# Kernel tuning notes

Hardware: AMD Instinct MI355X
Metric: run time of the kernel (lower is better)

The kernel has to match this reference:

```python
import jax, jax.numpy as jnp
import numpy as np

N_NODES = 50000


def setup_inputs() -> dict:
    key = jax.random.key(0)
    k1, k2, k3, k4, k5 = jax.random.split(key, 5)
    N, E, D_IN, D_OUT = N_NODES, 800000, 128, 128
    features = jax.random.normal(k1, (N, D_IN), dtype=jnp.float32)
    src = jax.random.randint(k2, (E,), 0, N, dtype=jnp.int32)
    dst = jax.random.randint(k3, (E,), 0, N, dtype=jnp.int32)
    # Kaiming-ish init for linear weights
    W_self = jax.random.normal(k4, (D_IN, D_OUT), dtype=jnp.float32) / np.sqrt(D_IN)
    W_neigh = jax.random.normal(k5, (D_IN, D_OUT), dtype=jnp.float32) / np.sqrt(D_IN)
    b = jnp.zeros((D_OUT,), dtype=jnp.float32)
    return {"features": features, "src": src, "dst": dst,
            "W_self": W_self, "W_neigh": W_neigh, "b": b}


def reference(features, src, dst, W_self, W_neigh, b):
    # DGL SAGEConv with 'mean' aggregator:
    #   h_neigh[v] = mean_{(u->v) in E} features[u]   (0 if in-degree 0)
    #   out = features @ W_self + h_neigh @ W_neigh + b
    N = features.shape[0]
    # gather source features along edges, then segment-sum into destinations
    neigh_sum = jax.ops.segment_sum(features[src], dst, num_segments=N)  # [N, D]
    deg = jax.ops.segment_sum(jnp.ones_like(dst, dtype=features.dtype), dst,
                              num_segments=N)  # [N]
    h_neigh = neigh_sum / jnp.maximum(deg, 1.0)[:, None]
    return features @ W_self + h_neigh @ W_neigh + b
```

## Files before the change

kernel.cpp:

```cpp
#include <hip/hip_runtime.h>

#define D 128
#define CAPN 64
#define HPAD 136
#define EC 2048
#define BSH 8
#define CAP 5120
#define CSTR 16

typedef __attribute__((ext_vector_type(8))) short bf16x8;
typedef __attribute__((ext_vector_type(4))) float f32x4;
typedef __attribute__((ext_vector_type(2))) float f32x2;

__device__ __forceinline__ unsigned short f2bf(float f) {
    union { float f; unsigned int u; } c;
    c.f = f;
    unsigned int lsb = (c.u >> 16) & 1u;
    c.u += 0x7fffu + lsb;
    return (unsigned short)(c.u >> 16);
}

__device__ __forceinline__ float bf_lo(unsigned int x) {
    union { unsigned int u; float f; } c;
    c.u = x << 16;
    return c.f;
}
__device__ __forceinline__ float bf_hi(unsigned int x) {
    union { unsigned int u; float f; } c;
    c.u = x & 0xffff0000u;
    return c.f;
}

__global__ __launch_bounds__(256) void prep_kernel(const float* __restrict__ feat,
                                                   unsigned short* __restrict__ fb,
                                                   unsigned char* __restrict__ fq,
                                                   const float* __restrict__ Ws,
                                                   const float* __restrict__ Wn,
                                                   unsigned short* __restrict__ Wfrag,
                                                   int* __restrict__ bin_cursor,
                                                   int castB, int n8, int N) {
    int bid = blockIdx.x;
    int t   = threadIdx.x;
    if (bid < castB) {
        int i = bid * 256 + t;
        if (i >= n8) return;
        const float4* s = (const float4*)(feat + (size_t)i * 8);
        float4 a = s[0];
        float4 b = s[1];
        unsigned short pk[8];
        pk[0] = f2bf(a.x); pk[1] = f2bf(a.y); pk[2] = f2bf(a.z); pk[3] = f2bf(a.w);
        pk[4] = f2bf(b.x); pk[5] = f2bf(b.y); pk[6] = f2bf(b.z); pk[7] = f2bf(b.w);
        *(bf16x8*)(fb + (size_t)i * 8) = *(const bf16x8*)pk;
        unsigned int q0 = __builtin_amdgcn_cvt_pk_fp8_f32(a.x, a.y, 0u, false);
        q0 = __builtin_amdgcn_cvt_pk_fp8_f32(a.z, a.w, q0, true);
        unsigned int q1 = __builtin_amdgcn_cvt_pk_fp8_f32(b.x, b.y, 0u, false);
        q1 = __builtin_amdgcn_cvt_pk_fp8_f32(b.z, b.w, q1, true);
        uint2 qq; qq.x = q0; qq.y = q1;
        *(uint2*)(fq + (size_t)i * 8) = qq;
    } else if (bid < castB + 16) {
        int tid = (bid - castB) * 256 + t;
        int l  = tid & 63;
        int ks = (tid >> 6) & 7;
        int nt = tid >> 9;
        int n  = nt * 16 + (l & 15);
        int kb = ks * 32 + (l >> 4) * 8;
        unsigned short pk[8];
#pragma unroll
        for (int j = 0; j < 8; ++j) {
            int k = kb + j;
            float w = (k < 128) ? Ws[k * D + n] : Wn[(k - 128) * D + n];
            pk[j] = f2bf(w);
        }
        *(bf16x8*)(Wfrag + (size_t)tid * 8) = *(const bf16x8*)pk;
    } else {
#pragma unroll
        for (int j = 0; j < CSTR; ++j)
            bin_cursor[j * 256 + t] = 0;
        if (t < 64)
            ((unsigned int*)(fb + (size_t)N * D))[t] = 0;
        if (t < 32)
            ((unsigned int*)(fq + (size_t)N * D))[t] = 0;
    }
}

__global__ __launch_bounds__(256) void binscatter_kernel(const int* __restrict__ src,
                                                         const int* __restrict__ dst,
                                                         int* __restrict__ bin_cursor,
                                                         unsigned int* __restrict__ ebuf,
                                                         int E, int NB) {
    __shared__ int cnt[256];
    __shared__ int basev[256];
    __shared__ int cur[256];
    int t = threadIdx.x;
    cnt[t] = 0;
    cur[t] = 0;
    __syncthreads();
    int base = blockIdx.x * EC;
    int dr[EC / 256];
#pragma unroll
    for (int i = 0; i < EC / 256; ++i) {
        int e = base + i * 256 + t;
        dr[i] = (e < E) ? dst[e] : -1;
        if (dr[i] >= 0) atomicAdd(&cnt[dr[i] >> BSH], 1);
    }
    __syncthreads();
    if (t < NB && cnt[t]) basev[t] = atomicAdd(&bin_cursor[t * CSTR], cnt[t]);
    __syncthreads();
#pragma unroll
    for (int i = 0; i < EC / 256; ++i) {
        int e = base + i * 256 + t;
        if (dr[i] >= 0) {
            int d = dr[i];
            int b = d >> BSH;
            int loc = basev[b] + atomicAdd(&cur[b], 1);
            if (loc < CAP)
                ebuf[(size_t)b * CAP + loc] =
                    (unsigned int)src[e] | ((unsigned int)(d & ((1 << BSH) - 1)) << 16);
        }
    }
}

__global__ __launch_bounds__(256) void csrbin_kernel(const unsigned int* __restrict__ ebuf,
                                                     const int* __restrict__ bin_cursor,
                                                     int* __restrict__ deg_g,
                                                     unsigned short* __restrict__ bucket,
                                                     int N) {
    __shared__ unsigned short lb[256 * CAPN];
    __shared__ int degL[256];
    int b = blockIdx.x;
    int t = threadIdx.x;
    int cntb = bin_cursor[b * CSTR];
    if (cntb > CAP) cntb = CAP;
    int s  = b * CAP;
    int e2 = s + cntb;

    degL[t] = 0;
    __syncthreads();

    for (int i = s + t; i < e2; i += 256) {
        unsigned int p = ebuf[i];
        int dl = (p >> 16) & 255;
        int slot = atomicAdd(&degL[dl], 1);
        if (slot < CAPN)
            lb[dl * CAPN + slot] = (unsigned short)(p & 0xffffu);
    }
    __syncthreads();

    int node = (b << BSH) + t;
    if (node < N) deg_g[node] = degL[t];

    uint4* dstq = (uint4*)(bucket + (size_t)b * 256 * CAPN);
    const uint4* srcq = (const uint4*)lb;
#pragma unroll
    for (int k = 0; k < (256 * CAPN) / 8 / 256; ++k)
        dstq[k * 256 + t] = srcq[k * 256 + t];
}

__global__ __launch_bounds__(256) void gather_mfma_kernel(
        const unsigned short* __restrict__ fb,
        const unsigned char* __restrict__ fq,
        const unsigned short* __restrict__ bucket,
        const int* __restrict__ deg,
        const unsigned short* __restrict__ Wfrag,
        const float* __restrict__ bias,
        float* __restrict__ out, int N) {
    __shared__ unsigned short hL[16 * HPAD];

    int t    = threadIdx.x;
    int w    = t >> 6;
    int lane = t & 63;
    int half = lane >> 5;
    int c32  = lane & 31;
    int lo16 = lane & 15;
    int quad = lane >> 4;
    int v0   = blockIdx.x * 16;
    int n0   = v0 + w * 4;

    int rowA = v0 + lo16;
    if (rowA > N - 1) rowA = N - 1;
    bf16x8 aself[4];
#pragma unroll
    for (int ks = 0; ks < 4; ++ks)
        aself[ks] = *(const bf16x8*)(fb + (size_t)rowA * D + ks * 32 + quad * 8);

    int nd = n0 + (lane & 3);
    int dn = (nd < N) ? deg[nd] : 0;
    int idx0 = (n0 + 0 < N) ? (int)bucket[(size_t)(n0 + 0) * CAPN + lane] : 0;
    int idx1 = (n0 + 1 < N) ? (int)bucket[(size_t)(n0 + 1) * CAPN + lane] : 0;
    int idx2 = (n0 + 2 < N) ? (int)bucket[(size_t)(n0 + 2) * CAPN + lane] : 0;
    int idx3 = (n0 + 3 < N) ? (int)bucket[(size_t)(n0 + 3) * CAPN + lane] : 0;

    int dt0 = __shfl(dn, 0), dt1 = __shfl(dn, 1);
    int dt2 = __shfl(dn, 2), dt3 = __shfl(dn, 3);
    int d0 = (n0 + 0 < N) ? ((dt0 > CAPN) ? CAPN : dt0) : 0;
    int d1 = (n0 + 1 < N) ? ((dt1 > CAPN) ? CAPN : dt1) : 0;
    int d2 = (n0 + 2 < N) ? ((dt2 > CAPN) ? CAPN : dt2) : 0;
    int d3 = (n0 + 3 < N) ? ((dt3 > CAPN) ? CAPN : dt3) : 0;

    unsigned int xA[16], xB[16];

#define ISSUE(X, idxreg, dd, e0)                                              \
    {                                                                         \
        _Pragma("unroll")                                                     \
        for (int j = 0; j < 16; ++j) {                                        \
            int sl = __builtin_amdgcn_readlane(idxreg, (e0) + 2 * j);         \
            int sh = __builtin_amdgcn_readlane(idxreg, (e0) + 2 * j + 1);     \
            sl = ((e0) + 2 * j     < (dd)) ? sl : N;                          \
            sh = ((e0) + 2 * j + 1 < (dd)) ? sh : N;                          \
            int ue = half ? sh : sl;                                          \
            X[j] = *(const unsigned int*)(fq + (size_t)ue * D + c32 * 4);     \
        }                                                                     \
    }

#define ACCUM(X)                                                              \
    {                                                                         \
        _Pragma("unroll")                                                     \
        for (int j = 0; j < 16; ++j) {                                        \
            f32x2 lo = __builtin_amdgcn_cvt_pk_f32_fp8(X[j], false);          \
            f32x2 hi = __builtin_amdgcn_cvt_pk_f32_fp8(X[j], true);           \
            a0 += lo.x; a1 += lo.y; a2 += hi.x; a3 += hi.y;                   \
        }                                                                     \
    }

#define FINISH(X, idxreg, dd, dtrue, nn)                                      \
    {                                                                         \
        float a0 = 0.f, a1 = 0.f, a2 = 0.f, a3 = 0.f;                         \
        ACCUM(X);                                                             \
        for (int e0 = 32; e0 < (dd); e0 += 32) {                              \
            ISSUE(X, idxreg, dd, e0);                                         \
            ACCUM(X);                                                         \
        }                                                                     \
        a0 += __shfl_xor(a0, 32);                                             \
        a1 += __shfl_xor(a1, 32);                                             \
        a2 += __shfl_xor(a2, 32);                                             \
        a3 += __shfl_xor(a3, 32);                                             \
        if (lane < 32) {                                                      \
            float inv = ((dd) > 0) ? 1.0f / (float)(dtrue) : 0.0f;            \
            uint2 pk;                                                         \
            pk.x = ((unsigned int)f2bf(a1 * inv) << 16) | f2bf(a0 * inv);     \
            pk.y = ((unsigned int)f2bf(a3 * inv) << 16) | f2bf(a2 * inv);     \
            *(uint2*)&hL[(w * 4 + (nn)) * HPAD + c32 * 4] = pk;               \
        }                                                                     \
    }

    ISSUE(xA, idx0, d0, 0);
    ISSUE(xB, idx1, d1, 0);
    FINISH(xA, idx0, d0, dt0, 0);
    ISSUE(xA, idx2, d2, 0);
    FINISH(xB, idx1, d1, dt1, 1);
    ISSUE(xB, idx3, d3, 0);
    FINISH(xA, idx2, d2, dt2, 2);
    FINISH(xB, idx3, d3, dt3, 3);

#undef ISSUE
#undef ACCUM
#undef FINISH

    __syncthreads();

    f32x4 accO[2];
#pragma unroll
    for (int ntl = 0; ntl < 2; ++ntl) accO[ntl] = (f32x4){0.f, 0.f, 0.f, 0.f};

#pragma unroll
    for (int ks = 0; ks < 8; ++ks) {
        bf16x8 a;
        if (ks < 4)
            a = aself[ks];
        else
            a = *(const bf16x8*)&hL[lo16 * HPAD + (ks - 4) * 32 + quad * 8];
        const unsigned short* wp = Wfrag + ((size_t)ks * 64 + lane) * 8;
#pragma unroll
        for (int ntl = 0; ntl < 2; ++ntl) {
            int nt = w * 2 + ntl;
            bf16x8 b = *(const bf16x8*)(wp + (size_t)nt * 4096);
            accO[ntl] = __builtin_amdgcn_mfma_f32_16x16x32_bf16(a, b, accO[ntl], 0, 0, 0);
        }
    }

#pragma unroll
    for (int ntl = 0; ntl < 2; ++ntl) {
        int n = (w * 2 + ntl) * 16 + lo16;
        float bvl = bias[n];
#pragma unroll
        for (int r = 0; r < 4; ++r) {
            int row = v0 + quad * 4 + r;
            if (row < N) out[(size_t)row * D + n] = accO[ntl][r] + bvl;
        }
    }
}

extern "C" void kernel_launch(void* const* d_in, const int* in_sizes, int n_in,
                              void* d_out, int out_size, void* d_ws, size_t ws_size,
                              hipStream_t stream) {
    const float* feat = (const float*)d_in[0];
    const int*   src  = (const int*)d_in[1];
    const int*   dst  = (const int*)d_in[2];
    const float* Ws   = (const float*)d_in[3];
    const float* Wn   = (const float*)d_in[4];
    const float* bias = (const float*)d_in[5];
    float*       out  = (float*)d_out;

    const int N  = in_sizes[0] / D;
    const int E  = in_sizes[1];
    const int NB = (N + (1 << BSH) - 1) >> BSH;
    const int nchunk = (E + EC - 1) / EC;
    const int castB  = (N * D / 8 + 255) / 256;

    int* bin_cursor = (int*)d_ws;
    int* deg        = bin_cursor + 256 * CSTR;
    unsigned int* ebuf = (unsigned int*)(deg + N);
    unsigned short* bucket = (unsigned short*)(ebuf + (size_t)NB * CAP);
    size_t short_count = (size_t)NB * 256 * CAPN;
    short_count = (short_count + 7) & ~(size_t)7;
    unsigned short* fb    = bucket + short_count;
    unsigned short* Wfrag = fb + (size_t)(N + 1) * D;
    unsigned char*  fq    = (unsigned char*)(Wfrag + 32768);

    prep_kernel<<<castB + 17, 256, 0, stream>>>(feat, fb, fq, Ws, Wn, Wfrag, bin_cursor,
                                                castB, N * D / 8, N);
    binscatter_kernel<<<nchunk, 256, 0, stream>>>(src, dst, bin_cursor, ebuf, E, NB);
    csrbin_kernel<<<NB, 256, 0, stream>>>(ebuf, bin_cursor, deg, bucket, N);
    gather_mfma_kernel<<<(N + 15) / 16, 256, 0, stream>>>(fb, fq, bucket, deg, Wfrag,
                                                          bias, out, N);
}
```

Before: 149.3 us.

## Fuse binning into prep kernel and switch buckets to compact CSR layout

Merges the edge bin-scatter into the feature-cast prep kernel as extra blocks, and moves the bin-cursor reset into a memset so the two can run in one launch. The CSR-build kernel now does a count pass plus a prefix scan and writes neighbor indices compactly with per-node row starts, instead of fixed 64-slot padded buckets. This shrinks the bucket write/read footprint and LDS use. The gather reads row starts via shuffle and accumulates fp8 conversions in packed float2 vectors. Risks: an extra pass over ebuf, the scan's barrier cost, and reading past a node's segment, which stays harmless because of the degree masking.

```diff
diff --git a/kernel.cpp b/kernel.cpp
--- a/kernel.cpp
+++ b/kernel.cpp
@@ -20,25 +20,21 @@
     return (unsigned short)(c.u >> 16);
 }
 
-__device__ __forceinline__ float bf_lo(unsigned int x) {
-    union { unsigned int u; float f; } c;
-    c.u = x << 16;
-    return c.f;
-}
-__device__ __forceinline__ float bf_hi(unsigned int x) {
-    union { unsigned int u; float f; } c;
-    c.u = x & 0xffff0000u;
-    return c.f;
-}
-
-__global__ __launch_bounds__(256) void prep_kernel(const float* __restrict__ feat,
-                                                   unsigned short* __restrict__ fb,
-                                                   unsigned char* __restrict__ fq,
-                                                   const float* __restrict__ Ws,
-                                                   const float* __restrict__ Wn,
-                                                   unsigned short* __restrict__ Wfrag,
-                                                   int* __restrict__ bin_cursor,
-                                                   int castB, int n8, int N) {
+__global__ __launch_bounds__(256) void prep_bins_kernel(const float* __restrict__ feat,
+                                                        unsigned short* __restrict__ fb,
+                                                        unsigned char* __restrict__ fq,
+                                                        const float* __restrict__ Ws,
+                                                        const float* __restrict__ Wn,
+                                                        unsigned short* __restrict__ Wfrag,
+                                                        int* __restrict__ bin_cursor,
+                                                        const int* __restrict__ src,
+                                                        const int* __restrict__ dst,
+                                                        unsigned int* __restrict__ ebuf,
+                                                        int castB, int n8, int N,
+                                                        int E, int NB) {
+    __shared__ int cnt[256];
+    __shared__ int basev[256];
+    __shared__ int cur[256];
     int bid = blockIdx.x;
     int t   = threadIdx.x;
     if (bid < castB) {
@@ -72,61 +68,51 @@
             pk[j] = f2bf(w);
         }
         *(bf16x8*)(Wfrag + (size_t)tid * 8) = *(const bf16x8*)pk;
-    } else {
-#pragma unroll
-        for (int j = 0; j < CSTR; ++j)
-            bin_cursor[j * 256 + t] = 0;
+    } else if (bid == castB + 16) {
         if (t < 64)
             ((unsigned int*)(fb + (size_t)N * D))[t] = 0;
         if (t < 32)
             ((unsigned int*)(fq + (size_t)N * D))[t] = 0;
-    }
-}
-
-__global__ __launch_bounds__(256) void binscatter_kernel(const int* __restrict__ src,
-                                                         const int* __restrict__ dst,
-                                                         int* __restrict__ bin_cursor,
-                                                         unsigned int* __restrict__ ebuf,
-                                                         int E, int NB) {
-    __shared__ int cnt[256];
-    __shared__ int basev[256];
-    __shared__ int cur[256];
-    int t = threadIdx.x;
-    cnt[t] = 0;
-    cur[t] = 0;
-    __syncthreads();
-    int base = blockIdx.x * EC;
-    int dr[EC / 256];
-#pragma unroll
-    for (int i = 0; i < EC / 256; ++i) {
-        int e = base + i * 256 + t;
-        dr[i] = (e < E) ? dst[e] : -1;
-        if (dr[i] >= 0) atomicAdd(&cnt[dr[i] >> BSH], 1);
-    }
-    __syncthreads();
-    if (t < NB && cnt[t]) basev[t] = atomicAdd(&bin_cursor[t * CSTR], cnt[t]);
-    __syncthreads();
-#pragma unroll
-    for (int i = 0; i < EC / 256; ++i) {
-        int e = base + i * 256 + t;
-        if (dr[i] >= 0) {
-            int d = dr[i];
-            int b = d >> BSH;
-            int loc = basev[b] + atomicAdd(&cur[b], 1);
-            if (loc < CAP)
-                ebuf[(size_t)b * CAP + loc] =
-                    (unsigned int)src[e] | ((unsigned int)(d & ((1 << BSH) - 1)) << 16);
+    } else {
+        cnt[t] = 0;
+        cur[t] = 0;
+        __syncthreads();
+        int base = (bid - castB - 17) * EC;
+        int dr[EC / 256];
+#pragma unroll
+        for (int i = 0; i < EC / 256; ++i) {
+            int e = base + i * 256 + t;
+            dr[i] = (e < E) ? dst[e] : -1;
+            if (dr[i] >= 0) atomicAdd(&cnt[dr[i] >> BSH], 1);
+        }
+        __syncthreads();
+        if (t < NB && cnt[t]) basev[t] = atomicAdd(&bin_cursor[t * CSTR], cnt[t]);
+        __syncthreads();
+#pragma unroll
+        for (int i = 0; i < EC / 256; ++i) {
+            int e = base + i * 256 + t;
+            if (dr[i] >= 0) {
+                int d = dr[i];
+                int b = d >> BSH;
+                int loc = basev[b] + atomicAdd(&cur[b], 1);
+                if (loc < CAP)
+                    ebuf[(size_t)b * CAP + loc] =
+                        (unsigned int)src[e] | ((unsigned int)(d & ((1 << BSH) - 1)) << 16);
+            }
         }
     }
 }
 
 __global__ __launch_bounds__(256) void csrbin_kernel(const unsigned int* __restrict__ ebuf,
                                                      const int* __restrict__ bin_cursor,
+                                                     int* __restrict__ rs_g,
                                                      int* __restrict__ deg_g,
                                                      unsigned short* __restrict__ bucket,
                                                      int N) {
-    __shared__ unsigned short lb[256 * CAPN];
+    __shared__ unsigned short lb[CAP];
     __shared__ int degL[256];
+    __shared__ int scn[256];
+    __shared__ int cur[256];
     int b = blockIdx.x;
     int t = threadIdx.x;
     int cntb = bin_cursor[b * CSTR];
@@ -135,31 +121,47 @@
     int e2 = s + cntb;
 
     degL[t] = 0;
-    __syncthreads();
+    cur[t]  = 0;
+    __syncthreads();
+    for (int i = s + t; i < e2; i += 256)
+        atomicAdd(&degL[(ebuf[i] >> 16) & 255], 1);
+    __syncthreads();
+
+    scn[t] = degL[t];
+    __syncthreads();
+    for (int off = 1; off < 256; off <<= 1) {
+        int add = (t >= off) ? scn[t - off] : 0;
+        __syncthreads();
+        scn[t] += add;
+        __syncthreads();
+    }
 
     for (int i = s + t; i < e2; i += 256) {
         unsigned int p = ebuf[i];
         int dl = (p >> 16) & 255;
-        int slot = atomicAdd(&degL[dl], 1);
-        if (slot < CAPN)
-            lb[dl * CAPN + slot] = (unsigned short)(p & 0xffffu);
+        int sl = atomicAdd(&cur[dl], 1);
+        lb[(scn[dl] - degL[dl]) + sl] = (unsigned short)(p & 0xffffu);
     }
     __syncthreads();
 
     int node = (b << BSH) + t;
-    if (node < N) deg_g[node] = degL[t];
-
-    uint4* dstq = (uint4*)(bucket + (size_t)b * 256 * CAPN);
-    const uint4* srcq = (const uint4*)lb;
-#pragma unroll
-    for (int k = 0; k < (256 * CAPN) / 8 / 256; ++k)
-        dstq[k * 256 + t] = srcq[k * 256 + t];
+    if (node < N) {
+        rs_g[node]  = s + scn[t] - degL[t];
+        deg_g[node] = degL[t];
+    }
+
+    int nq = (cntb + 7) >> 3;
+    uint4* dq = (uint4*)(bucket + (size_t)s);
+    const uint4* sq = (const uint4*)lb;
+    for (int k = t; k < nq; k += 256)
+        dq[k] = sq[k];
 }
 
 __global__ __launch_bounds__(256) void gather_mfma_kernel(
         const unsigned short* __restrict__ fb,
         const unsigned char* __restrict__ fq,
         const unsigned short* __restrict__ bucket,
+        const int* __restrict__ rs,
         const int* __restrict__ deg,
         const unsigned short* __restrict__ Wfrag,
         const float* __restrict__ bias,
@@ -184,11 +186,16 @@
         aself[ks] = *(const bf16x8*)(fb + (size_t)rowA * D + ks * 32 + quad * 8);
 
     int nd = n0 + (lane & 3);
-    int dn = (nd < N) ? deg[nd] : 0;
-    int idx0 = (n0 + 0 < N) ? (int)bucket[(size_t)(n0 + 0) * CAPN + lane] : 0;
-    int idx1 = (n0 + 1 < N) ? (int)bucket[(size_t)(n0 + 1) * CAPN + lane] : 0;
-    int idx2 = (n0 + 2 < N) ? (int)bucket[(size_t)(n0 + 2) * CAPN + lane] : 0;
-    int idx3 = (n0 + 3 < N) ? (int)bucket[(size_t)(n0 + 3) * CAPN + lane] : 0;
+    int ok = (nd < N);
+    int dn = ok ? deg[nd] : 0;
+    int rn = ok ? rs[nd] : 0;
+
+    int r0 = __shfl(rn, 0), r1 = __shfl(rn, 1);
+    int r2 = __shfl(rn, 2), r3 = __shfl(rn, 3);
+    int idx0 = (n0 + 0 < N) ? (int)bucket[(size_t)r0 + lane] : 0;
+    int idx1 = (n0 + 1 < N) ? (int)bucket[(size_t)r1 + lane] : 0;
+    int idx2 = (n0 + 2 < N) ? (int)bucket[(size_t)r2 + lane] : 0;
+    int idx3 = (n0 + 3 < N) ? (int)bucket[(size_t)r3 + lane] : 0;
 
     int dt0 = __shfl(dn, 0), dt1 = __shfl(dn, 1);
     int dt2 = __shfl(dn, 2), dt3 = __shfl(dn, 3);
@@ -216,20 +223,21 @@
     {                                                                         \
         _Pragma("unroll")                                                     \
         for (int j = 0; j < 16; ++j) {                                        \
-            f32x2 lo = __builtin_amdgcn_cvt_pk_f32_fp8(X[j], false);          \
-            f32x2 hi = __builtin_amdgcn_cvt_pk_f32_fp8(X[j], true);           \
-            a0 += lo.x; a1 += lo.y; a2 += hi.x; a3 += hi.y;                   \
+            s01 += __builtin_amdgcn_cvt_pk_f32_fp8(X[j], false);              \
+            s23 += __builtin_amdgcn_cvt_pk_f32_fp8(X[j], true);               \
         }                                                                     \
     }
 
 #define FINISH(X, idxreg, dd, dtrue, nn)                                      \
     {                                                                         \
-        float a0 = 0.f, a1 = 0.f, a2 = 0.f, a3 = 0.f;                         \
+        f32x2 s01 = (f32x2){0.f, 0.f};                                        \
+        f32x2 s23 = (f32x2){0.f, 0.f};                                        \
         ACCUM(X);                                                             \
         for (int e0 = 32; e0 < (dd); e0 += 32) {                              \
             ISSUE(X, idxreg, dd, e0);                                         \
             ACCUM(X);                                                         \
         }                                                                     \
+        float a0 = s01.x, a1 = s01.y, a2 = s23.x, a3 = s23.y;                 \
         a0 += __shfl_xor(a0, 32);                                             \
         a1 += __shfl_xor(a1, 32);                                             \
         a2 += __shfl_xor(a2, 32);                                             \
@@ -308,19 +316,21 @@
     const int castB  = (N * D / 8 + 255) / 256;
 
     int* bin_cursor = (int*)d_ws;
-    int* deg        = bin_cursor + 256 * CSTR;
+    int* rs         = bin_cursor + 256 * CSTR;
+    int* deg        = rs + N;
     unsigned int* ebuf = (unsigned int*)(deg + N);
     unsigned short* bucket = (unsigned short*)(ebuf + (size_t)NB * CAP);
-    size_t short_count = (size_t)NB * 256 * CAPN;
+    size_t short_count = (size_t)NB * CAP + 64;
     short_count = (short_count + 7) & ~(size_t)7;
     unsigned short* fb    = bucket + short_count;
     unsigned short* Wfrag = fb + (size_t)(N + 1) * D;
     unsigned char*  fq    = (unsigned char*)(Wfrag + 32768);
 
-    prep_kernel<<<castB + 17, 256, 0, stream>>>(feat, fb, fq, Ws, Wn, Wfrag, bin_cursor,
-                                                castB, N * D / 8, N);
-    binscatter_kernel<<<nchunk, 256, 0, stream>>>(src, dst, bin_cursor, ebuf, E, NB);
-    csrbin_kernel<<<NB, 256, 0, stream>>>(ebuf, bin_cursor, deg, bucket, N);
-    gather_mfma_kernel<<<(N + 15) / 16, 256, 0, stream>>>(fb, fq, bucket, deg, Wfrag,
-                                                          bias, out, N);
-}
+    hipMemsetAsync(bin_cursor, 0, 256 * CSTR * sizeof(int), stream);
+    prep_bins_kernel<<<castB + 17 + nchunk, 256, 0, stream>>>(
+        feat, fb, fq, Ws, Wn, Wfrag, bin_cursor, src, dst, ebuf,
+        castB, N * D / 8, N, E, NB);
+    csrbin_kernel<<<NB, 256, 0, stream>>>(ebuf, bin_cursor, rs, deg, bucket, N);
+    gather_mfma_kernel<<<(N + 15) / 16, 256, 0, stream>>>(fb, fq, bucket, rs, deg,
+                                                          Wfrag, bias, out, N);
+}
```

After: 151.7 us. No clear change (+1.6%).
